# Performance work log

Hardware: AMD Instinct MI355X
Metric: run time of the kernel (lower is better)

Reference implementation:

```python
import jax, jax.numpy as jnp
import numpy as np

B, N, E, F, H = 4, 10000, 320000, 128, 128


def setup_inputs() -> dict:
    key = jax.random.key(0)
    ks = jax.random.split(key, 12)
    s = 1.0 / np.sqrt(F)
    sh = 1.0 / np.sqrt(H)
    return {
        "batch_feat": jax.random.normal(ks[0], (B, N, F), dtype=jnp.float32),
        "batch_edges": jax.random.randint(ks[1], (B, 2, E), 0, N, dtype=jnp.int32),
        "batch_attr": jax.random.uniform(ks[2], (B, E), dtype=jnp.float32),
        "W1": jax.random.uniform(ks[3], (F, H), jnp.float32, -s, s),
        "b1": jnp.zeros((H,), jnp.float32),
        "W2": jax.random.uniform(ks[4], (H, H), jnp.float32, -sh, sh),
        "b2": jnp.zeros((H,), jnp.float32),
        "W3": jax.random.uniform(ks[5], (H, H), jnp.float32, -sh, sh),
        "b3": jnp.zeros((H,), jnp.float32),
        "Wl": jax.random.uniform(ks[6], (H, 1), jnp.float32, -sh, sh),
        "bl": jnp.zeros((1,), jnp.float32),
    }


def reference(batch_feat, batch_edges, batch_attr, W1, b1, W2, b2, W3, b3, Wl, bl):
    n_nodes = batch_feat.shape[1]

    def gcn_conv(x, row, col, w, W, b):
        # PyG gcn_norm with add_self_loops=False: deg = scatter_add(w, col)
        deg = jax.ops.segment_sum(w, col, num_segments=n_nodes)  # [N]
        dinv = jnp.where(deg > 0, jax.lax.rsqrt(deg), 0.0)
        norm = dinv[row] * w * dinv[col]                         # [E]
        xw = x @ W                                               # [N,H]
        msg = norm[:, None] * xw[row]                            # gather [E,H]
        return jax.ops.segment_sum(msg, col, num_segments=n_nodes) + b

    def per_graph(x, ei, w):
        row, col = ei[0], ei[1]
        h = jax.nn.relu(gcn_conv(x, row, col, w, W1, b1))
        h = jax.nn.relu(gcn_conv(h, row, col, w, W2, b2))
        h = jax.nn.relu(gcn_conv(h, row, col, w, W3, b3))
        return h.mean(axis=0) @ Wl + bl                          # [1]

    return jax.vmap(per_graph)(batch_feat, batch_edges, batch_attr)  # [B,1]
```

## Files before the change

### kernel.cpp

```cpp
#include <hip/hip_runtime.h>

#define BB 4
#define NN 10000
#define EE 320000
#define HH 128
#define HALFN 5000
#define NK2 (2 * NN)
#define RS (2 * NN + 1)
#define NHB 64
#define EPB (EE / NHB)

__global__ __launch_bounds__(256) void hist_kernel(
    const int* __restrict__ edges, int* __restrict__ hb,
    unsigned short* __restrict__ lrank) {
  __shared__ int lh[NN];
  int b = blockIdx.y;
  int blk = blockIdx.x;
  int t = threadIdx.x;
  const int* rows = edges + (size_t)b * 2 * EE;
  const int* cols = rows + EE;
#pragma unroll
  for (int half = 0; half < 2; ++half) {
    for (int i = t; i < NN; i += 256) lh[i] = 0;
    __syncthreads();
    for (int i = t; i < EPB; i += 256) {
      int e = blk * EPB + i;
      int row = rows[e];
      int col = cols[e];
      if ((row >= HALFN) == (half != 0)) {
        int lr = atomicAdd(&lh[col], 1);
        lrank[(size_t)b * EE + e] = (unsigned short)lr;
      }
    }
    __syncthreads();
    int* hbrow = hb + ((size_t)(b * NHB + blk)) * NK2 + half * NN;
    for (int i = t; i < NN; i += 256) hbrow[i] = lh[i];
    __syncthreads();
  }
}

__global__ __launch_bounds__(256) void colscan_kernel(
    int* __restrict__ hb, int* __restrict__ cnt) {
  int b = blockIdx.y;
  int k = blockIdx.x * 256 + threadIdx.x;
  if (k >= NK2) return;
  int acc = 0;
  for (int j = 0; j < NHB; ++j) {
    size_t idx = ((size_t)(b * NHB + j)) * NK2 + k;
    int v = hb[idx];
    hb[idx] = acc;
    acc += v;
  }
  cnt[b * NK2 + k] = acc;
}

__global__ __launch_bounds__(256) void scan_kernel(
    const int* __restrict__ cnt, int* __restrict__ rowstart) {
  int b = blockIdx.x, t = threadIdx.x;
  __shared__ int s[256];
  int running = 0;
  for (int base = 0; base < NK2; base += 2048) {
    int v[8];
    int i0 = base + t * 8;
    int tsum = 0;
#pragma unroll
    for (int j = 0; j < 8; ++j) {
      v[j] = (i0 + j < NK2) ? cnt[b * NK2 + i0 + j] : 0;
      tsum += v[j];
    }
    s[t] = tsum;
    __syncthreads();
    for (int o = 1; o < 256; o <<= 1) {
      int add = (t >= o) ? s[t - o] : 0;
      __syncthreads();
      s[t] += add;
      __syncthreads();
    }
    int ex = running + s[t] - tsum;
#pragma unroll
    for (int j = 0; j < 8; ++j) {
      if (i0 + j < NK2) rowstart[b * RS + i0 + j] = ex;
      ex += v[j];
    }
    int tot = s[255];
    __syncthreads();
    running += tot;
  }
  if (t == 0) rowstart[b * RS + NK2] = running;
}

__global__ __launch_bounds__(256) void fill_kernel(
    const int* __restrict__ edges, const float* __restrict__ attr,
    const unsigned short* __restrict__ lrank, const int* __restrict__ hb,
    const int* __restrict__ rowstart, int2* __restrict__ csr) {
  int b = blockIdx.y;
  int e0 = (blockIdx.x * 256 + threadIdx.x) * 2;
  int blk = e0 / EPB;
  int2 rr = *(const int2*)(edges + (size_t)b * 2 * EE + e0);
  int2 cc = *(const int2*)(edges + (size_t)b * 2 * EE + EE + e0);
  float2 ww = *(const float2*)(attr + (size_t)b * EE + e0);
  unsigned int lr2 = *(const unsigned int*)(lrank + (size_t)b * EE + e0);
  int k0 = ((rr.x >= HALFN) ? NN : 0) + cc.x;
  int k1 = ((rr.y >= HALFN) ? NN : 0) + cc.y;
  const int* hbrow = hb + ((size_t)(b * NHB + blk)) * NK2;
  int p0 = rowstart[b * RS + k0] + hbrow[k0] + (int)(lr2 & 0xffffu);
  int p1 = rowstart[b * RS + k1] + hbrow[k1] + (int)(lr2 >> 16);
  csr[(size_t)b * EE + p0] = make_int2(rr.x, __float_as_int(ww.x));
  csr[(size_t)b * EE + p1] = make_int2(rr.y, __float_as_int(ww.y));
}

__global__ __launch_bounds__(256) void deg_kernel(
    const int2* __restrict__ csr, const int* __restrict__ rowstart,
    float* __restrict__ dinv) {
  int b = blockIdx.y;
  int n = blockIdx.x * 256 + threadIdx.x;
  if (n >= NN) return;
  const int2* c = csr + (size_t)b * EE;
  float sum = 0.f;
#pragma unroll
  for (int q = 0; q < 2; ++q) {
    int key = q * NN + n;
    int s0 = rowstart[b * RS + key], s1 = rowstart[b * RS + key + 1];
    for (int i = s0; i < s1; ++i) sum += __int_as_float(c[i].y);
  }
  dinv[b * NN + n] = sum > 0.f ? rsqrtf(sum) : 0.f;
}

__global__ __launch_bounds__(256) void gemm_kernel(
    const float* __restrict__ x, const float* __restrict__ W,
    float* __restrict__ out) {
  __shared__ float xs[32 * 68];
  __shared__ float ws[32 * 144];
  int b = blockIdx.y;
  int row0 = blockIdx.x * 64;
  int t = threadIdx.x;
  int rg = t >> 4, cg = t & 15;
  int fc = cg * 8 + ((cg >> 2) << 2);
  float acc[4][8];
#pragma unroll
  for (int r = 0; r < 4; ++r)
#pragma unroll
    for (int j = 0; j < 8; ++j) acc[r][j] = 0.f;
  const float* xb = x + (size_t)b * NN * HH;

  for (int k0 = 0; k0 < HH; k0 += 32) {
#pragma unroll
    for (int i = 0; i < 2; ++i) {
      int idx = t + i * 256;
      int rl = idx >> 3, kq = idx & 7;
      int row = row0 + rl;
      float4 v = make_float4(0.f, 0.f, 0.f, 0.f);
      if (row < NN) v = *(const float4*)(xb + (size_t)row * HH + k0 + kq * 4);
      xs[(kq * 4 + 0) * 68 + rl] = v.x;
      xs[(kq * 4 + 1) * 68 + rl] = v.y;
      xs[(kq * 4 + 2) * 68 + rl] = v.z;
      xs[(kq * 4 + 3) * 68 + rl] = v.w;
    }
#pragma unroll
    for (int i = 0; i < 4; ++i) {
      int idx = t + i * 256;
      int kk = idx >> 5, c = (idx & 31) * 4;
      float4 v = *(const float4*)(W + (size_t)(k0 + kk) * HH + c);
      int f = c + ((c >> 5) << 2);
      *(float4*)&ws[kk * 144 + f] = v;
    }
    __syncthreads();
#pragma unroll 4
    for (int k = 0; k < 32; ++k) {
      float4 xv = *(const float4*)&xs[k * 68 + rg * 4];
      float4 w0 = *(const float4*)&ws[k * 144 + fc];
      float4 w1 = *(const float4*)&ws[k * 144 + fc + 4];
      const float* xp = (const float*)&xv;
#pragma unroll
      for (int r = 0; r < 4; ++r) {
        acc[r][0] += xp[r] * w0.x; acc[r][1] += xp[r] * w0.y;
        acc[r][2] += xp[r] * w0.z; acc[r][3] += xp[r] * w0.w;
        acc[r][4] += xp[r] * w1.x; acc[r][5] += xp[r] * w1.y;
        acc[r][6] += xp[r] * w1.z; acc[r][7] += xp[r] * w1.w;
      }
    }
    __syncthreads();
  }
#pragma unroll
  for (int r = 0; r < 4; ++r) {
    int row = row0 + rg * 4 + r;
    if (row < NN) {
      float* og = out + ((size_t)b * NN + row) * HH + cg * 8;
      *(float4*)og = make_float4(acc[r][0], acc[r][1], acc[r][2], acc[r][3]);
      *(float4*)(og + 4) = make_float4(acc[r][4], acc[r][5], acc[r][6], acc[r][7]);
    }
  }
}

__global__ __launch_bounds__(256) void agg_kernel(
    const float* __restrict__ xw, const int2* __restrict__ csr,
    const int* __restrict__ rowstart, const float* __restrict__ dinv,
    const float* __restrict__ bias, float* __restrict__ h, int phase) {
  int g = blockIdx.x & 7;
  int b = g >> 1;
  int q = g & 1;
  int chunk = blockIdx.x >> 3;
  int nhalf = (phase == 0) ? q : 1 - q;
  int half = (threadIdx.x >> 5) & 1;
  int n = nhalf * HALFN + chunk * 8 + (threadIdx.x >> 6) * 2 + half;
  int sl = threadIdx.x & 31;
  int key = q * NN + n;
  int s0 = rowstart[b * RS + key], s1 = rowstart[b * RS + key + 1];
  const float* xwg = xw + (size_t)b * NN * HH;
  const float* dv = dinv + b * NN;
  const int2* c = csr + (size_t)b * EE;
  float4 a0 = make_float4(0.f, 0.f, 0.f, 0.f);
  float4 a1 = make_float4(0.f, 0.f, 0.f, 0.f);
  float4 a2 = make_float4(0.f, 0.f, 0.f, 0.f);
  float4 a3 = make_float4(0.f, 0.f, 0.f, 0.f);
  int i = s0;
  for (; i + 4 <= s1; i += 4) {
    int2 e0 = c[i];
    int2 e1 = c[i + 1];
    int2 e2 = c[i + 2];
    int2 e3 = c[i + 3];
    float w0 = __int_as_float(e0.y) * dv[e0.x];
    float w1 = __int_as_float(e1.y) * dv[e1.x];
    float w2 = __int_as_float(e2.y) * dv[e2.x];
    float w3 = __int_as_float(e3.y) * dv[e3.x];
    float4 v0 = *(const float4*)(xwg + (size_t)e0.x * HH + sl * 4);
    float4 v1 = *(const float4*)(xwg + (size_t)e1.x * HH + sl * 4);
    float4 v2 = *(const float4*)(xwg + (size_t)e2.x * HH + sl * 4);
    float4 v3 = *(const float4*)(xwg + (size_t)e3.x * HH + sl * 4);
    a0.x += w0 * v0.x; a0.y += w0 * v0.y; a0.z += w0 * v0.z; a0.w += w0 * v0.w;
    a1.x += w1 * v1.x; a1.y += w1 * v1.y; a1.z += w1 * v1.z; a1.w += w1 * v1.w;
    a2.x += w2 * v2.x; a2.y += w2 * v2.y; a2.z += w2 * v2.z; a2.w += w2 * v2.w;
    a3.x += w3 * v3.x; a3.y += w3 * v3.y; a3.z += w3 * v3.z; a3.w += w3 * v3.w;
  }
  for (; i < s1; ++i) {
    int2 e0 = c[i];
    float w0 = __int_as_float(e0.y) * dv[e0.x];
    float4 v0 = *(const float4*)(xwg + (size_t)e0.x * HH + sl * 4);
    a0.x += w0 * v0.x; a0.y += w0 * v0.y; a0.z += w0 * v0.z; a0.w += w0 * v0.w;
  }
  a0.x += a1.x + a2.x + a3.x;
  a0.y += a1.y + a2.y + a3.y;
  a0.z += a1.z + a2.z + a3.z;
  a0.w += a1.w + a2.w + a3.w;
  float* hp = h + ((size_t)b * NN + n) * HH + sl * 4;
  if (phase == 0) {
    *(float4*)hp = a0;
  } else {
    float dn = dv[n];
    float4 prev = *(const float4*)hp;
    float4 bb = *(const float4*)(bias + sl * 4);
    *(float4*)hp = make_float4(fmaxf((prev.x + a0.x) * dn + bb.x, 0.f),
                               fmaxf((prev.y + a0.y) * dn + bb.y, 0.f),
                               fmaxf((prev.z + a0.z) * dn + bb.z, 0.f),
                               fmaxf((prev.w + a0.w) * dn + bb.w, 0.f));
  }
}

__global__ __launch_bounds__(64) void init_out_kernel(float* out, const float* __restrict__ bl) {
  if (threadIdx.x < BB) out[threadIdx.x] = bl[0];
}

__global__ __launch_bounds__(256) void final_kernel(
    const float* __restrict__ h, const float* __restrict__ Wl,
    float* __restrict__ out) {
  int b = blockIdx.y;
  int t = threadIdx.x;
  int f = t & 127;
  int rr = t >> 7;
  float p = 0.f;
  for (int n = blockIdx.x * 2 + rr; n < NN; n += gridDim.x * 2)
    p += h[((size_t)b * NN + n) * HH + f];
  __shared__ float s[256];
  s[t] = p;
  __syncthreads();
  float v = 0.f;
  if (t < 128) v = (s[t] + s[t + 128]) * Wl[f];
  __syncthreads();
  s[t] = v;
  __syncthreads();
  for (int o = 64; o > 0; o >>= 1) {
    if (t < o) s[t] += s[t + o];
    __syncthreads();
  }
  if (t == 0) atomicAdd(&out[b], s[0] * (1.0f / NN));
}

extern "C" void kernel_launch(void* const* d_in, const int* in_sizes, int n_in,
                              void* d_out, int out_size, void* d_ws, size_t ws_size,
                              hipStream_t stream) {
  const float* feat = (const float*)d_in[0];
  const int* edges = (const int*)d_in[1];
  const float* attr = (const float*)d_in[2];
  const float* W1 = (const float*)d_in[3];
  const float* b1 = (const float*)d_in[4];
  const float* W2 = (const float*)d_in[5];
  const float* b2 = (const float*)d_in[6];
  const float* W3 = (const float*)d_in[7];
  const float* b3 = (const float*)d_in[8];
  const float* Wl = (const float*)d_in[9];
  const float* bl = (const float*)d_in[10];
  float* out = (float*)d_out;

  char* ws = (char*)d_ws;
  size_t off = 0;
  auto alloc = [&](size_t bytes) {
    size_t o = off;
    off = (off + bytes + 255) & ~(size_t)255;
    return o;
  };
  int*   cnt      = (int*)  (ws + alloc((size_t)BB * NK2 * 4));
  int*   rowstart = (int*)  (ws + alloc((size_t)BB * RS * 4));
  int2*  csr      = (int2*) (ws + alloc((size_t)BB * EE * 8));
  float* xw       = (float*)(ws + alloc((size_t)BB * NN * HH * 4));
  float* h        = (float*)(ws + alloc((size_t)BB * NN * HH * 4));
  unsigned short* lrank = (unsigned short*)xw;
  int*   hb   = (int*)h;
  float* dinv = (float*)cnt;

  dim3 hgrid(NHB, BB);
  hist_kernel<<<hgrid, 256, 0, stream>>>(edges, hb, lrank);
  colscan_kernel<<<dim3((NK2 + 255) / 256, BB), 256, 0, stream>>>(hb, cnt);
  scan_kernel<<<BB, 256, 0, stream>>>(cnt, rowstart);
  dim3 egrid2(EE / 512, BB);
  fill_kernel<<<egrid2, 256, 0, stream>>>(edges, attr, lrank, hb, rowstart, csr);
  deg_kernel<<<dim3((NN + 255) / 256, BB), 256, 0, stream>>>(csr, rowstart, dinv);

  dim3 ggrid((NN + 63) / 64, BB);
  int agrid = 8 * (HALFN / 8);

  gemm_kernel<<<ggrid, 256, 0, stream>>>(feat, W1, xw);
  agg_kernel<<<agrid, 256, 0, stream>>>(xw, csr, rowstart, dinv, b1, h, 0);
  agg_kernel<<<agrid, 256, 0, stream>>>(xw, csr, rowstart, dinv, b1, h, 1);
  gemm_kernel<<<ggrid, 256, 0, stream>>>(h, W2, xw);
  agg_kernel<<<agrid, 256, 0, stream>>>(xw, csr, rowstart, dinv, b2, h, 0);
  agg_kernel<<<agrid, 256, 0, stream>>>(xw, csr, rowstart, dinv, b2, h, 1);
  gemm_kernel<<<ggrid, 256, 0, stream>>>(h, W3, xw);
  agg_kernel<<<agrid, 256, 0, stream>>>(xw, csr, rowstart, dinv, b3, h, 0);
  agg_kernel<<<agrid, 256, 0, stream>>>(xw, csr, rowstart, dinv, b3, h, 1);

  init_out_kernel<<<1, 64, 0, stream>>>(out, bl);
  final_kernel<<<dim3(64, BB), 256, 0, stream>>>(h, Wl, out);
}
```

Before: 373.3 us.

## Merge split aggregation passes into one launch and fuse epilogue into next GEMM

The two sequential aggregation launches per layer (one per source-row half) are replaced by a single launch covering both halves. Each half writes its partial sum to its own buffer. The normalization, bias and ReLU epilogue moves into the next GEMM's load stage and into the final mean reduction, so the read-modify-write of h is gone. The block histogram buffer also shrinks from int to ushort. In exchange there is an extra full-size partial buffer, each later consumer reads two partial arrays, and the split that kept each half's source rows cache-local within one launch is lost.

After: 347.0 us. -7.1%, faster.

```diff
diff --git a/kernel.cpp b/kernel.cpp
--- a/kernel.cpp
+++ b/kernel.cpp
@@ -11,7 +11,7 @@
 #define EPB (EE / NHB)
 
 __global__ __launch_bounds__(256) void hist_kernel(
-    const int* __restrict__ edges, int* __restrict__ hb,
+    const int* __restrict__ edges, unsigned short* __restrict__ hb,
     unsigned short* __restrict__ lrank) {
   __shared__ int lh[NN];
   int b = blockIdx.y;
@@ -33,14 +33,14 @@
       }
     }
     __syncthreads();
-    int* hbrow = hb + ((size_t)(b * NHB + blk)) * NK2 + half * NN;
-    for (int i = t; i < NN; i += 256) hbrow[i] = lh[i];
+    unsigned short* hbrow = hb + ((size_t)(b * NHB + blk)) * NK2 + half * NN;
+    for (int i = t; i < NN; i += 256) hbrow[i] = (unsigned short)lh[i];
     __syncthreads();
   }
 }
 
 __global__ __launch_bounds__(256) void colscan_kernel(
-    int* __restrict__ hb, int* __restrict__ cnt) {
+    unsigned short* __restrict__ hb, int* __restrict__ cnt) {
   int b = blockIdx.y;
   int k = blockIdx.x * 256 + threadIdx.x;
   if (k >= NK2) return;
@@ -48,7 +48,7 @@
   for (int j = 0; j < NHB; ++j) {
     size_t idx = ((size_t)(b * NHB + j)) * NK2 + k;
     int v = hb[idx];
-    hb[idx] = acc;
+    hb[idx] = (unsigned short)acc;
     acc += v;
   }
   cnt[b * NK2 + k] = acc;
@@ -91,7 +91,7 @@
 
 __global__ __launch_bounds__(256) void fill_kernel(
     const int* __restrict__ edges, const float* __restrict__ attr,
-    const unsigned short* __restrict__ lrank, const int* __restrict__ hb,
+    const unsigned short* __restrict__ lrank, const unsigned short* __restrict__ hb,
     const int* __restrict__ rowstart, int2* __restrict__ csr) {
   int b = blockIdx.y;
   int e0 = (blockIdx.x * 256 + threadIdx.x) * 2;
@@ -102,9 +102,9 @@
   unsigned int lr2 = *(const unsigned int*)(lrank + (size_t)b * EE + e0);
   int k0 = ((rr.x >= HALFN) ? NN : 0) + cc.x;
   int k1 = ((rr.y >= HALFN) ? NN : 0) + cc.y;
-  const int* hbrow = hb + ((size_t)(b * NHB + blk)) * NK2;
-  int p0 = rowstart[b * RS + k0] + hbrow[k0] + (int)(lr2 & 0xffffu);
-  int p1 = rowstart[b * RS + k1] + hbrow[k1] + (int)(lr2 >> 16);
+  const unsigned short* hbrow = hb + ((size_t)(b * NHB + blk)) * NK2;
+  int p0 = rowstart[b * RS + k0] + (int)hbrow[k0] + (int)(lr2 & 0xffffu);
+  int p1 = rowstart[b * RS + k1] + (int)hbrow[k1] + (int)(lr2 >> 16);
   csr[(size_t)b * EE + p0] = make_int2(rr.x, __float_as_int(ww.x));
   csr[(size_t)b * EE + p1] = make_int2(rr.y, __float_as_int(ww.y));
 }
@@ -127,8 +127,10 @@
 }
 
 __global__ __launch_bounds__(256) void gemm_kernel(
-    const float* __restrict__ x, const float* __restrict__ W,
-    float* __restrict__ out) {
+    const float* __restrict__ xsrc, const float* __restrict__ p0,
+    const float* __restrict__ p1, const float* __restrict__ dinv,
+    const float* __restrict__ xbias, const float* __restrict__ W,
+    float* __restrict__ out, int fused) {
   __shared__ float xs[32 * 68];
   __shared__ float ws[32 * 144];
   int b = blockIdx.y;
@@ -141,7 +143,7 @@
   for (int r = 0; r < 4; ++r)
 #pragma unroll
     for (int j = 0; j < 8; ++j) acc[r][j] = 0.f;
-  const float* xb = x + (size_t)b * NN * HH;
+  size_t gbase = (size_t)b * NN * HH;
 
   for (int k0 = 0; k0 < HH; k0 += 32) {
 #pragma unroll
@@ -150,7 +152,21 @@
       int rl = idx >> 3, kq = idx & 7;
       int row = row0 + rl;
       float4 v = make_float4(0.f, 0.f, 0.f, 0.f);
-      if (row < NN) v = *(const float4*)(xb + (size_t)row * HH + k0 + kq * 4);
+      if (row < NN) {
+        size_t o = gbase + (size_t)row * HH + k0 + kq * 4;
+        if (fused) {
+          float4 u0 = *(const float4*)(p0 + o);
+          float4 u1 = *(const float4*)(p1 + o);
+          float dn = dinv[b * NN + row];
+          float4 bb = *(const float4*)(xbias + k0 + kq * 4);
+          v.x = fmaxf((u0.x + u1.x) * dn + bb.x, 0.f);
+          v.y = fmaxf((u0.y + u1.y) * dn + bb.y, 0.f);
+          v.z = fmaxf((u0.z + u1.z) * dn + bb.z, 0.f);
+          v.w = fmaxf((u0.w + u1.w) * dn + bb.w, 0.f);
+        } else {
+          v = *(const float4*)(xsrc + o);
+        }
+      }
       xs[(kq * 4 + 0) * 68 + rl] = v.x;
       xs[(kq * 4 + 1) * 68 + rl] = v.y;
       xs[(kq * 4 + 2) * 68 + rl] = v.z;
@@ -185,7 +201,7 @@
   for (int r = 0; r < 4; ++r) {
     int row = row0 + rg * 4 + r;
     if (row < NN) {
-      float* og = out + ((size_t)b * NN + row) * HH + cg * 8;
+      float* og = out + gbase + (size_t)row * HH + cg * 8;
       *(float4*)og = make_float4(acc[r][0], acc[r][1], acc[r][2], acc[r][3]);
       *(float4*)(og + 4) = make_float4(acc[r][4], acc[r][5], acc[r][6], acc[r][7]);
     }
@@ -195,14 +211,13 @@
 __global__ __launch_bounds__(256) void agg_kernel(
     const float* __restrict__ xw, const int2* __restrict__ csr,
     const int* __restrict__ rowstart, const float* __restrict__ dinv,
-    const float* __restrict__ bias, float* __restrict__ h, int phase) {
+    float* __restrict__ p0g, float* __restrict__ p1g) {
   int g = blockIdx.x & 7;
   int b = g >> 1;
   int q = g & 1;
   int chunk = blockIdx.x >> 3;
-  int nhalf = (phase == 0) ? q : 1 - q;
   int half = (threadIdx.x >> 5) & 1;
-  int n = nhalf * HALFN + chunk * 8 + (threadIdx.x >> 6) * 2 + half;
+  int n = chunk * 8 + (threadIdx.x >> 6) * 2 + half;
   int sl = threadIdx.x & 31;
   int key = q * NN + n;
   int s0 = rowstart[b * RS + key], s1 = rowstart[b * RS + key + 1];
@@ -242,18 +257,8 @@
   a0.y += a1.y + a2.y + a3.y;
   a0.z += a1.z + a2.z + a3.z;
   a0.w += a1.w + a2.w + a3.w;
-  float* hp = h + ((size_t)b * NN + n) * HH + sl * 4;
-  if (phase == 0) {
-    *(float4*)hp = a0;
-  } else {
-    float dn = dv[n];
-    float4 prev = *(const float4*)hp;
-    float4 bb = *(const float4*)(bias + sl * 4);
-    *(float4*)hp = make_float4(fmaxf((prev.x + a0.x) * dn + bb.x, 0.f),
-                               fmaxf((prev.y + a0.y) * dn + bb.y, 0.f),
-                               fmaxf((prev.z + a0.z) * dn + bb.z, 0.f),
-                               fmaxf((prev.w + a0.w) * dn + bb.w, 0.f));
-  }
+  float* pq = (q == 0) ? p0g : p1g;
+  *(float4*)(pq + ((size_t)b * NN + n) * HH + sl * 4) = a0;
 }
 
 __global__ __launch_bounds__(64) void init_out_kernel(float* out, const float* __restrict__ bl) {
@@ -261,15 +266,20 @@
 }
 
 __global__ __launch_bounds__(256) void final_kernel(
-    const float* __restrict__ h, const float* __restrict__ Wl,
-    float* __restrict__ out) {
+    const float* __restrict__ p0g, const float* __restrict__ p1g,
+    const float* __restrict__ dinv, const float* __restrict__ b3,
+    const float* __restrict__ Wl, float* __restrict__ out) {
   int b = blockIdx.y;
   int t = threadIdx.x;
   int f = t & 127;
   int rr = t >> 7;
+  float bf = b3[f];
+  const float* dv = dinv + b * NN;
   float p = 0.f;
-  for (int n = blockIdx.x * 2 + rr; n < NN; n += gridDim.x * 2)
-    p += h[((size_t)b * NN + n) * HH + f];
+  for (int n = blockIdx.x * 2 + rr; n < NN; n += gridDim.x * 2) {
+    size_t o = ((size_t)b * NN + n) * HH + f;
+    p += fmaxf((p0g[o] + p1g[o]) * dv[n] + bf, 0.f);
+  }
   __shared__ float s[256];
   s[t] = p;
   __syncthreads();
@@ -312,9 +322,10 @@
   int*   rowstart = (int*)  (ws + alloc((size_t)BB * RS * 4));
   int2*  csr      = (int2*) (ws + alloc((size_t)BB * EE * 8));
   float* xw       = (float*)(ws + alloc((size_t)BB * NN * HH * 4));
-  float* h        = (float*)(ws + alloc((size_t)BB * NN * HH * 4));
+  float* p0       = (float*)(ws + alloc((size_t)BB * NN * HH * 4));
+  float* p1       = (float*)(ws + alloc((size_t)BB * NN * HH * 4));
   unsigned short* lrank = (unsigned short*)xw;
-  int*   hb   = (int*)h;
+  unsigned short* hb    = (unsigned short*)p0;
   float* dinv = (float*)cnt;
 
   dim3 hgrid(NHB, BB);
@@ -326,18 +337,15 @@
   deg_kernel<<<dim3((NN + 255) / 256, BB), 256, 0, stream>>>(csr, rowstart, dinv);
 
   dim3 ggrid((NN + 63) / 64, BB);
-  int agrid = 8 * (HALFN / 8);
-
-  gemm_kernel<<<ggrid, 256, 0, stream>>>(feat, W1, xw);
-  agg_kernel<<<agrid, 256, 0, stream>>>(xw, csr, rowstart, dinv, b1, h, 0);
-  agg_kernel<<<agrid, 256, 0, stream>>>(xw, csr, rowstart, dinv, b1, h, 1);
-  gemm_kernel<<<ggrid, 256, 0, stream>>>(h, W2, xw);
-  agg_kernel<<<agrid, 256, 0, stream>>>(xw, csr, rowstart, dinv, b2, h, 0);
-  agg_kernel<<<agrid, 256, 0, stream>>>(xw, csr, rowstart, dinv, b2, h, 1);
-  gemm_kernel<<<ggrid, 256, 0, stream>>>(h, W3, xw);
-  agg_kernel<<<agrid, 256, 0, stream>>>(xw, csr, rowstart, dinv, b3, h, 0);
-  agg_kernel<<<agrid, 256, 0, stream>>>(xw, csr, rowstart, dinv, b3, h, 1);
+  int agrid = 8 * (NN / 8);
+
+  gemm_kernel<<<ggrid, 256, 0, stream>>>(feat, nullptr, nullptr, nullptr, nullptr, W1, xw, 0);
+  agg_kernel<<<agrid, 256, 0, stream>>>(xw, csr, rowstart, dinv, p0, p1);
+  gemm_kernel<<<ggrid, 256, 0, stream>>>(nullptr, p0, p1, dinv, b1, W2, xw, 1);
+  agg_kernel<<<agrid, 256, 0, stream>>>(xw, csr, rowstart, dinv, p0, p1);
+  gemm_kernel<<<ggrid, 256, 0, stream>>>(nullptr, p0, p1, dinv, b2, W3, xw, 1);
+  agg_kernel<<<agrid, 256, 0, stream>>>(xw, csr, rowstart, dinv, p0, p1);
 
   init_out_kernel<<<1, 64, 0, stream>>>(out, bl);
-  final_kernel<<<dim3(64, BB), 256, 0, stream>>>(h, Wl, out);
-}
+  final_kernel<<<dim3(64, BB), 256, 0, stream>>>(p0, p1, dinv, b3, Wl, out);
+}
```
